# Optimization experiments

Hardware: AMD Instinct MI355X
Metric: run time of the kernel (lower is better)

## Reference

```python
import jax, jax.numpy as jnp
import numpy as np

B, T, V, D, P, DEP = 64, 32, 32000, 1024, 8, 4
TAU = 1.0
EPS = 1e-5


def setup_inputs() -> dict:
    key = jax.random.key(0)
    ks = jax.random.split(key, 9)
    s = 0.02
    x = jax.random.randint(ks[0], (B, T), 0, V)
    emb = jax.random.normal(ks[1], (V, D), jnp.float32) * s
    pos = jax.random.normal(ks[2], (T, D), jnp.float32) * s
    # primitive library: n_prims MLPs (Linear -> GELU -> Linear), stacked
    w1 = jax.random.normal(ks[3], (P, D, D), jnp.float32) * s
    b1 = jnp.zeros((P, D), jnp.float32)
    w2 = jax.random.normal(ks[4], (P, D, D), jnp.float32) * s
    b2 = jnp.zeros((P, D), jnp.float32)
    # one selector Linear(dim, n_prims) per depth
    sel_w = jax.random.normal(ks[5], (DEP, P, D), jnp.float32) * s
    sel_b = jnp.zeros((DEP, P), jnp.float32)
    ln_g = jnp.ones((D,), jnp.float32)
    ln_b = jnp.zeros((D,), jnp.float32)
    head_w = jax.random.normal(ks[6], (V, D), jnp.float32) * s
    # fixed gumbel noise (replaces torch's in-op sampling, kept deterministic)
    u = jax.random.uniform(ks[7], (DEP, B, P), jnp.float32, 1e-6, 1.0 - 1e-6)
    gumbel = -jnp.log(-jnp.log(u))
    return dict(x=x, emb=emb, pos=pos, w1=w1, b1=b1, w2=w2, b2=b2,
                sel_w=sel_w, sel_b=sel_b, ln_g=ln_g, ln_b=ln_b,
                head_w=head_w, gumbel=gumbel)


def reference(x, emb, pos, w1, b1, w2, b2, sel_w, sel_b, ln_g, ln_b, head_w, gumbel):
    h = emb[x] + pos[None, :x.shape[1], :]          # [B,T,D]
    div = jnp.float32(0.0)
    unif = jnp.float32(1.0 / P)
    for d in range(DEP):
        ctx = h.mean(axis=1)                         # [B,D]
        logits = ctx @ sel_w[d].T + sel_b[d]         # [B,P]
        weights = jax.nn.softmax((logits + gumbel[d]) / TAU, axis=-1)
        # all primitives over all tokens at once (grouped GEMM), no T loop
        u1 = jax.nn.gelu(jnp.einsum('btd,pde->btpe', h, w1) + b1, approximate=False)
        prim = jnp.einsum('btpe,pef->btpf', u1, w2) + b2   # [B,T,P,D]
        h = h + jnp.einsum('btpf,bp->btf', prim, weights)  # residual add
        avg = weights.mean(axis=0)                   # [P]
        # F.kl_div(avg.log(), uniform, reduction='sum')
        div = div + jnp.sum(unif * (jnp.log(unif) - jnp.log(avg)))
    mu = h.mean(-1, keepdims=True)
    var = ((h - mu) ** 2).mean(-1, keepdims=True)
    hn = (h - mu) * jax.lax.rsqrt(var + EPS) * ln_g + ln_b
    return hn @ head_w.T, div
```

## Files before the change

kernel.cpp:

```cpp
#include <hip/hip_runtime.h>
#include <hip/hip_bf16.h>
#include <math.h>

typedef __bf16 bf16x8 __attribute__((ext_vector_type(8)));
typedef float  f32x4  __attribute__((ext_vector_type(4)));

struct __align__(8) bf16x4s { __hip_bfloat16 a, b, c, d; };

__device__ __forceinline__ void gload_lds16(const void* g, void* l) {
  __builtin_amdgcn_global_load_lds(
      (const __attribute__((address_space(1))) void*)g,
      (__attribute__((address_space(3))) void*)l, 16, 0, 0);
}

__device__ __forceinline__ float fast_gelu(float v) {
  float s = 0.70710678118654752f * v;
  float a = fabsf(s);
  float t = __builtin_amdgcn_rcpf(fmaf(0.3275911f, a, 1.0f));
  float p = t * fmaf(t, fmaf(t, fmaf(t, fmaf(t, 1.061405429f, -1.453152027f),
                                     1.421413741f), -0.284496736f), 0.254829592f);
  float e = __expf(-a * a);
  float er = copysignf(fmaf(-p, e, 1.0f), s);
  return 0.5f * v * (1.0f + er);
}

#define BAR()   asm volatile("s_barrier" ::: "memory")
#define LGKM0() do { asm volatile("s_waitcnt lgkmcnt(0)" ::: "memory"); \
                     __builtin_amdgcn_sched_barrier(0); } while (0)
#define VMC(N)  do { asm volatile("s_waitcnt vmcnt(" #N ")" ::: "memory"); \
                     __builtin_amdgcn_sched_barrier(0); } while (0)
#define P1()    __builtin_amdgcn_s_setprio(1)
#define P0()    __builtin_amdgcn_s_setprio(0)

#define MQ(MB, NB, AV, BV)                                                    \
  do {                                                                        \
    _Pragma("unroll")                                                         \
    for (int mi_ = 0; mi_ < 4; ++mi_)                                         \
      _Pragma("unroll")                                                       \
      for (int nj_ = 0; nj_ < 2; ++nj_)                                       \
        _Pragma("unroll")                                                     \
        for (int kk_ = 0; kk_ < 2; ++kk_)                                     \
          acc[MB + mi_][NB + nj_] = __builtin_amdgcn_mfma_f32_16x16x32_bf16(  \
              AV[mi_][kk_], BV[nj_][kk_], acc[MB + mi_][NB + nj_], 0, 0, 0);  \
  } while (0)

template<int EPI>
__global__ __launch_bounds__(512, 2)
void gemm_nt(const __hip_bfloat16* __restrict__ A,
             const __hip_bfloat16* __restrict__ B,
             const int K, const int Kc, const int N,
             const float* __restrict__ p0,
             const float* __restrict__ p1,
             float* __restrict__ f32out,
             __hip_bfloat16* __restrict__ bfout)
{
  __shared__ __align__(16) __hip_bfloat16 lds[65536];

  const int tid = threadIdx.x;
  const int lane = tid & 63, wid = tid >> 6;
  const int l15 = lane & 15, l4 = lane >> 4;
  const int r8 = lane >> 3, blk = lane & 7;
  const int wm = wid >> 2, wn = wid & 3;

  const int nx = gridDim.x;
  const int flat = blockIdx.x + nx * blockIdx.y;
  const int q = (nx * gridDim.y) >> 3;
  const int nid = (flat & 7) * q + (flat >> 3);
  const long m0 = (long)(nid % nx) * 256;
  const long n0 = (long)(nid / nx) * 256;

  const int kbeg = blockIdx.z * Kc;
  const int nt = Kc / 64;

  f32x4 acc[8][4] = {};
  bf16x8 arE[4][2], arL[4][2], brE[2][2], brL[2][2];

  auto stageA = [&](int buf, int h, int k0) {
#pragma unroll
    for (int p2 = 0; p2 < 2; ++p2) {
      int ch = p2 * 16 + h * 8 + wid;
      int row = ch * 8 + r8;
      gload_lds16(A + (m0 + row) * (long)K + k0 + ((blk ^ r8) << 3),
                  lds + buf * 16384 + ch * 512);
    }
  };
  auto stageB = [&](int buf, int h, int k0) {
#pragma unroll
    for (int p2 = 0; p2 < 2; ++p2) {
      int ch = (p2 * 2 + (wid >> 2)) * 8 + h * 4 + (wid & 3);
      int row = ch * 8 + r8;
      gload_lds16(B + (n0 + row) * (long)K + k0 + ((blk ^ r8) << 3),
                  lds + 32768 + buf * 16384 + ch * 512);
    }
  };
  auto stage4 = [&](int buf, int k0) {
    stageA(buf, 0, k0); stageA(buf, 1, k0);
    stageB(buf, 0, k0); stageB(buf, 1, k0);
  };
  auto readAE = [&](int buf) {
    const __hip_bfloat16* pA = lds + buf * 16384;
#pragma unroll
    for (int mi = 0; mi < 4; ++mi)
#pragma unroll
      for (int kk = 0; kk < 2; ++kk) {
        int row = wm * 128 + mi * 16 + l15;
        arE[mi][kk] = *(const bf16x8*)(pA + row * 64 + (((kk * 4 + l4) ^ (row & 7)) << 3));
      }
  };
  auto readAL = [&](int buf) {
    const __hip_bfloat16* pA = lds + buf * 16384;
#pragma unroll
    for (int mi = 0; mi < 4; ++mi)
#pragma unroll
      for (int kk = 0; kk < 2; ++kk) {
        int row = wm * 128 + 64 + mi * 16 + l15;
        arL[mi][kk] = *(const bf16x8*)(pA + row * 64 + (((kk * 4 + l4) ^ (row & 7)) << 3));
      }
  };
  auto readBE = [&](int buf) {
    const __hip_bfloat16* pB = lds + 32768 + buf * 16384;
#pragma unroll
    for (int nj = 0; nj < 2; ++nj)
#pragma unroll
      for (int kk = 0; kk < 2; ++kk) {
        int row = wn * 64 + nj * 16 + l15;
        brE[nj][kk] = *(const bf16x8*)(pB + row * 64 + (((kk * 4 + l4) ^ (row & 7)) << 3));
      }
  };
  auto readBL = [&](int buf) {
    const __hip_bfloat16* pB = lds + 32768 + buf * 16384;
#pragma unroll
    for (int nj = 0; nj < 2; ++nj)
#pragma unroll
      for (int kk = 0; kk < 2; ++kk) {
        int row = wn * 64 + 32 + nj * 16 + l15;
        brL[nj][kk] = *(const bf16x8*)(pB + row * 64 + (((kk * 4 + l4) ^ (row & 7)) << 3));
      }
  };

  stage4(0, kbeg);
  stage4(1, kbeg + 64);
  VMC(8);
  BAR();
  readAE(0); readBE(0);

  for (int s = 0; s < nt; ++s) {
    const int b = s & 1;
    readBL(b); readAL(b);
    P1();
    MQ(0, 0, arE, brE);
    MQ(0, 2, arE, brL);
    MQ(4, 0, arL, brE);
    MQ(4, 2, arL, brL);
    P0();
    LGKM0();
    BAR();
    if (s + 2 < nt) {
      stage4(b, kbeg + (s + 2) * 64);
      VMC(8);
    } else if (s + 2 == nt) {
      VMC(0);
    }
    BAR();
    if (s + 1 < nt) { readAE(b ^ 1); readBE(b ^ 1); }
  }

  const long slab = (EPI == 2) ? (long)blockIdx.z * (long)(gridDim.x * 256) * N : 0;
#pragma unroll
  for (int mi = 0; mi < 8; ++mi) {
    const long gmb = m0 + wm * 128 + mi * 16 + l4 * 4;
    const int b = (int)(gmb >> 5);
#pragma unroll
    for (int nj = 0; nj < 4; ++nj) {
      const long gn = n0 + wn * 64 + nj * 16 + l15;
      if constexpr (EPI == 0) {
        const int p = (int)(gn >> 10), e = (int)(gn & 1023);
        const float bias = p0[(p << 10) + e];
        const float wpb = p1[(b << 3) + p];
#pragma unroll
        for (int r = 0; r < 4; ++r) {
          float v = fast_gelu(acc[mi][nj][r] + bias) * wpb;
          bfout[(gmb + r) * (long)N + gn] = __float2bfloat16(v);
        }
      } else {
#pragma unroll
        for (int r = 0; r < 4; ++r)
          f32out[slab + (gmb + r) * (long)N + gn] = acc[mi][nj][r];
      }
    }
  }
}

__global__ void cvt_bf16_k(const float* __restrict__ in, __hip_bfloat16* __restrict__ out, long n) {
  long i = ((long)blockIdx.x * blockDim.x + threadIdx.x) * 4;
  if (i >= n) return;
  float4 v = *(const float4*)(in + i);
  *(bf16x4s*)(out + i) = bf16x4s{__float2bfloat16(v.x), __float2bfloat16(v.y),
                                 __float2bfloat16(v.z), __float2bfloat16(v.w)};
}

__global__ void tconv_k(const float* __restrict__ in, __hip_bfloat16* __restrict__ out,
                        long in_bs, long out_rs, long out_bs) {
  __shared__ float tile[32][33];
  int p = blockIdx.z;
  int r0 = blockIdx.y * 32, c0 = blockIdx.x * 32;
  int tx = threadIdx.x, ty = threadIdx.y;
#pragma unroll
  for (int i = 0; i < 32; i += 8)
    tile[ty + i][tx] = in[(long)p * in_bs + (long)(r0 + ty + i) * 1024 + c0 + tx];
  __syncthreads();
#pragma unroll
  for (int i = 0; i < 32; i += 8)
    out[(long)(c0 + ty + i) * out_rs + (long)p * out_bs + (r0 + tx)] =
        __float2bfloat16(tile[tx][ty + i]);
}

__global__ void embed_k(const int* __restrict__ x, const float* __restrict__ emb,
                        const float* __restrict__ pos, float* __restrict__ h,
                        __hip_bfloat16* __restrict__ hb, float* __restrict__ divp) {
  int row = blockIdx.x;
  int t = row & 31;
  int c = threadIdx.x * 4;
  long tok = x[row];
  float4 e = *(const float4*)(emb + tok * 1024 + c);
  float4 q = *(const float4*)(pos + (long)t * 1024 + c);
  float4 v{e.x + q.x, e.y + q.y, e.z + q.z, e.w + q.w};
  *(float4*)(h + (long)row * 1024 + c) = v;
  *(bf16x4s*)(hb + (long)row * 1024 + c) =
      bf16x4s{__float2bfloat16(v.x), __float2bfloat16(v.y),
              __float2bfloat16(v.z), __float2bfloat16(v.w)};
  if (row == 0 && threadIdx.x == 0) *divp = 0.f;
}

__global__ void select_wb2_k(const float* __restrict__ h, const float* __restrict__ selw,
                             const float* __restrict__ selb, const float* __restrict__ gum,
                             const float* __restrict__ b2, float* __restrict__ W,
                             float* __restrict__ wb2, int dep) {
  int b = blockIdx.x, tid = threadIdx.x;
  int c = tid * 4;
  float4 s{0.f, 0.f, 0.f, 0.f};
  for (int t = 0; t < 32; ++t) {
    const float4 v = *(const float4*)(h + ((long)(b * 32 + t)) * 1024 + c);
    s.x += v.x; s.y += v.y; s.z += v.z; s.w += v.w;
  }
  float lp[8];
#pragma unroll
  for (int p = 0; p < 8; ++p) {
    const float4 w = *(const float4*)(selw + dep * 8192 + p * 1024 + c);
    lp[p] = (s.x * w.x + s.y * w.y + s.z * w.z + s.w * w.w) * (1.f / 32.f);
  }
  int lane = tid & 63, wid = tid >> 6;
#pragma unroll
  for (int p = 0; p < 8; ++p)
    for (int o = 32; o; o >>= 1) lp[p] += __shfl_down(lp[p], o);
  __shared__ float red[4][8];
  __shared__ float wsm[8];
  if (lane == 0) {
#pragma unroll
    for (int p = 0; p < 8; ++p) red[wid][p] = lp[p];
  }
  __syncthreads();
  if (tid == 0) {
    float lg[8], mx = -1e30f;
    for (int p = 0; p < 8; ++p) {
      lg[p] = red[0][p] + red[1][p] + red[2][p] + red[3][p]
            + selb[dep * 8 + p] + gum[dep * 512 + b * 8 + p];
      mx = fmaxf(mx, lg[p]);
    }
    float sm = 0.f;
    for (int p = 0; p < 8; ++p) { lg[p] = expf(lg[p] - mx); sm += lg[p]; }
    float inv = 1.f / sm;
    for (int p = 0; p < 8; ++p) { wsm[p] = lg[p] * inv; W[dep * 512 + b * 8 + p] = lg[p] * inv; }
  }
  __syncthreads();
  float4 a{0.f, 0.f, 0.f, 0.f};
#pragma unroll
  for (int p = 0; p < 8; ++p) {
    float wp = wsm[p];
    const float4 v = *(const float4*)(b2 + p * 1024 + c);
    a.x += wp * v.x; a.y += wp * v.y; a.z += wp * v.z; a.w += wp * v.w;
  }
  *(float4*)(wb2 + (long)b * 1024 + c) = a;
}

__global__ void h_update_k(const float* __restrict__ part, float* __restrict__ h,
                           const float* __restrict__ wb2, __hip_bfloat16* __restrict__ hb,
                           const float* __restrict__ Wd, float* __restrict__ divp) {
  int row = blockIdx.x;
  int c = threadIdx.x * 4;
  long idx = (long)row * 1024 + c;
  float4 a = *(const float4*)(h + idx);
  const float4 w = *(const float4*)(wb2 + (long)(row >> 5) * 1024 + c);
  a.x += w.x; a.y += w.y; a.z += w.z; a.w += w.w;
#pragma unroll
  for (int s = 0; s < 8; ++s) {
    const float4 v = *(const float4*)(part + (long)s * 2097152 + idx);
    a.x += v.x; a.y += v.y; a.z += v.z; a.w += v.w;
  }
  *(float4*)(h + idx) = a;
  *(bf16x4s*)(hb + idx) = bf16x4s{__float2bfloat16(a.x), __float2bfloat16(a.y),
                                  __float2bfloat16(a.z), __float2bfloat16(a.w)};
  if (blockIdx.x == 0 && threadIdx.x < 64) {
    float w8[8];
#pragma unroll
    for (int p = 0; p < 8; ++p) w8[p] = Wd[threadIdx.x * 8 + p];
#pragma unroll
    for (int p = 0; p < 8; ++p)
      for (int o = 32; o; o >>= 1) w8[p] += __shfl_down(w8[p], o);
    if (threadIdx.x == 0) {
      float d = *divp;
      const float u = 0.125f, lu = logf(0.125f);
#pragma unroll
      for (int p = 0; p < 8; ++p) d += u * (lu - logf(w8[p] * (1.f / 64.f)));
      *divp = d;
    }
  }
}

__global__ void ln_k(const float* __restrict__ h, const float* __restrict__ g,
                     const float* __restrict__ be, __hip_bfloat16* __restrict__ hnb,
                     const float* __restrict__ divp, float* __restrict__ divout) {
  int row = blockIdx.x, tid = threadIdx.x;
  int c = tid * 4;
  const float4 v = *(const float4*)(h + (long)row * 1024 + c);
  float s = v.x + v.y + v.z + v.w;
  float q = v.x * v.x + v.y * v.y + v.z * v.z + v.w * v.w;
  for (int o = 32; o; o >>= 1) { s += __shfl_down(s, o); q += __shfl_down(q, o); }
  __shared__ float red[16];
  int lane = tid & 63, wid = tid >> 6;
  if (lane == 0) { red[wid] = s; red[8 + wid] = q; }
  __syncthreads();
  if (tid == 0) {
    float S = red[0] + red[1] + red[2] + red[3];
    float Q = red[8] + red[9] + red[10] + red[11];
    float mu = S * (1.f / 1024.f);
    float var = Q * (1.f / 1024.f) - mu * mu;
    red[0] = mu; red[1] = rsqrtf(var + 1e-5f);
  }
  __syncthreads();
  float mu = red[0], rs = red[1];
  float4 gg = *(const float4*)(g + c), bb = *(const float4*)(be + c);
  *(bf16x4s*)(hnb + (long)row * 1024 + c) =
      bf16x4s{__float2bfloat16((v.x - mu) * rs * gg.x + bb.x),
              __float2bfloat16((v.y - mu) * rs * gg.y + bb.y),
              __float2bfloat16((v.z - mu) * rs * gg.z + bb.z),
              __float2bfloat16((v.w - mu) * rs * gg.w + bb.w)};
  if (row == 0 && tid == 0) *divout = *divp;
}

extern "C" void kernel_launch(void* const* d_in, const int* in_sizes, int n_in,
                              void* d_out, int out_size, void* d_ws, size_t ws_size,
                              hipStream_t stream) {
  (void)in_sizes; (void)n_in; (void)out_size; (void)ws_size;
  const int*   x     = (const int*)  d_in[0];
  const float* emb   = (const float*)d_in[1];
  const float* pos   = (const float*)d_in[2];
  const float* w1    = (const float*)d_in[3];
  const float* b1    = (const float*)d_in[4];
  const float* w2    = (const float*)d_in[5];
  const float* b2    = (const float*)d_in[6];
  const float* selw  = (const float*)d_in[7];
  const float* selb  = (const float*)d_in[8];
  const float* lng   = (const float*)d_in[9];
  const float* lnb   = (const float*)d_in[10];
  const float* headw = (const float*)d_in[11];
  const float* gum   = (const float*)d_in[12];
  float* out = (float*)d_out;

  char* ws = (char*)d_ws;
  __hip_bfloat16* w1t   = (__hip_bfloat16*)(ws);
  __hip_bfloat16* w2t   = (__hip_bfloat16*)(ws + 16777216);
  __hip_bfloat16* headb = (__hip_bfloat16*)(ws + 33554432);
  float*          h     = (float*)(ws + 99090432);
  __hip_bfloat16* hb    = (__hip_bfloat16*)(ws + 107479040);
  __hip_bfloat16* u1    = (__hip_bfloat16*)(ws + 111673344);
  float*          Wall  = (float*)(ws + 145227776);
  float*          wb2   = (float*)(ws + 145240064);
  float*          divp  = (float*)(ws + 145502208);
  float*          part  = out;

  cvt_bf16_k<<<32000, 256, 0, stream>>>(headw, headb, 32768000L);
  tconv_k<<<dim3(32, 32, 8), dim3(32, 8), 0, stream>>>(w1, w1t, 1L << 20, 1024L, 1L << 20);
  tconv_k<<<dim3(32, 32, 8), dim3(32, 8), 0, stream>>>(w2, w2t, 1L << 20, 8192L, 1024L);
  embed_k<<<2048, 256, 0, stream>>>(x, emb, pos, h, hb, divp);

  for (int d = 0; d < 4; ++d) {
    select_wb2_k<<<64, 256, 0, stream>>>(h, selw, selb, gum, b2, Wall, wb2, d);
    gemm_nt<0><<<dim3(8, 32), 512, 0, stream>>>(hb, w1t, 1024, 1024, 8192, b1, Wall + d * 512, nullptr, u1);
    gemm_nt<2><<<dim3(8, 4, 8), 512, 0, stream>>>(u1, w2t, 8192, 1024, 1024, nullptr, nullptr, part, nullptr);
    h_update_k<<<2048, 256, 0, stream>>>(part, h, wb2, hb, Wall + d * 512, divp);
  }

  ln_k<<<2048, 256, 0, stream>>>(h, lng, lnb, hb, divp, out + 65536000L);
  gemm_nt<2><<<dim3(8, 125), 512, 0, stream>>>(hb, headb, 1024, 1024, 32000, nullptr, nullptr, out, nullptr);
}
```

Before: 662.8 us.

## Interleave global-to-LDS staging with MFMA quadrants in an eight-phase unrolled loop

Restructures the GEMM main loop into a two-stage unrolled schedule. Each of the four MFMA quadrants is preceded by a fine-grained slice of the next tile's global-to-LDS loads and LDS reads, separated by barriers. The goal is to hide memory latency behind compute more evenly, in the style of hipBLASLt ping-pong schedules, instead of issuing all loads in one burst between compute blocks. It adds many more barriers and assumes nt is even, and the fine-grained buffer reuse ordering is easy to get wrong.

```diff
diff --git a/kernel.cpp b/kernel.cpp
--- a/kernel.cpp
+++ b/kernel.cpp
@@ -93,10 +93,6 @@
                   lds + 32768 + buf * 16384 + ch * 512);
     }
   };
-  auto stage4 = [&](int buf, int k0) {
-    stageA(buf, 0, k0); stageA(buf, 1, k0);
-    stageB(buf, 0, k0); stageB(buf, 1, k0);
-  };
   auto readAE = [&](int buf) {
     const __hip_bfloat16* pA = lds + buf * 16384;
 #pragma unroll
@@ -138,31 +134,58 @@
       }
   };
 
-  stage4(0, kbeg);
-  stage4(1, kbeg + 64);
-  VMC(8);
+  stageA(0, 0, kbeg); stageB(0, 0, kbeg); stageB(0, 1, kbeg); stageA(0, 1, kbeg);
+  VMC(4);
+  stageA(1, 0, kbeg + 64); stageB(1, 0, kbeg + 64); stageB(1, 1, kbeg + 64);
+  VMC(6);
   BAR();
-  readAE(0); readBE(0);
-
-  for (int s = 0; s < nt; ++s) {
-    const int b = s & 1;
-    readBL(b); readAL(b);
-    P1();
-    MQ(0, 0, arE, brE);
-    MQ(0, 2, arE, brL);
-    MQ(4, 0, arL, brE);
-    MQ(4, 2, arL, brL);
-    P0();
-    LGKM0();
-    BAR();
-    if (s + 2 < nt) {
-      stage4(b, kbeg + (s + 2) * 64);
-      VMC(8);
-    } else if (s + 2 == nt) {
-      VMC(0);
-    }
-    BAR();
-    if (s + 1 < nt) { readAE(b ^ 1); readBE(b ^ 1); }
+
+  const int nit = nt >> 1;
+  for (int t = 0; t < nit; ++t) {
+    const bool fl = (t + 1 < nit);
+    const int kA = kbeg + (2 * t + 1) * 64;
+    const int kB = kbeg + (2 * t + 2) * 64;
+    const int kC = kbeg + (2 * t + 3) * 64;
+    readAE(0); readBE(0);
+    stageA(1, 1, kA);
+    BAR(); LGKM0();
+    P1(); MQ(0, 0, arE, brE); P0();
+    BAR();
+    readBL(0);
+    if (fl) stageA(0, 0, kB);
+    BAR(); LGKM0();
+    P1(); MQ(0, 2, arE, brL); P0();
+    BAR();
+    readAL(0);
+    if (fl) stageB(0, 0, kB);
+    BAR(); LGKM0();
+    P1(); MQ(4, 0, arL, brE); P0();
+    BAR();
+    if (fl) stageB(0, 1, kB);
+    BAR();
+    P1(); MQ(4, 2, arL, brL); P0();
+    if (fl) { VMC(6); } else { VMC(0); }
+    BAR();
+    readAE(1); readBE(1);
+    if (fl) stageA(0, 1, kB);
+    BAR(); LGKM0();
+    P1(); MQ(0, 0, arE, brE); P0();
+    BAR();
+    readBL(1);
+    if (fl) stageA(1, 0, kC);
+    BAR(); LGKM0();
+    P1(); MQ(0, 2, arE, brL); P0();
+    BAR();
+    readAL(1);
+    if (fl) stageB(1, 0, kC);
+    BAR(); LGKM0();
+    P1(); MQ(4, 0, arL, brE); P0();
+    BAR();
+    if (fl) stageB(1, 1, kC);
+    BAR();
+    P1(); MQ(4, 2, arL, brL); P0();
+    if (fl) VMC(6);
+    BAR();
   }
 
   const long slab = (EPI == 2) ? (long)blockIdx.z * (long)(gridDim.x * 256) * N : 0;
```

Result: faster. 639.6 us (-3.5%).

## Load GEMM B operand directly to registers and store split-K partials in bf16

Applied to the files above, without the earlier changes.

The GEMM kernel now stages only the A tile through LDS, halving shared memory to 64KB. B fragments are loaded straight from global memory into double-buffered registers, and the K loop is unrolled by two. Split-K partial sums in the second MLP GEMM are written as bf16 instead of fp32, and h_update reads them as bf16, roughly halving that round-trip traffic. The cost is uncoalesced, per-lane global loads for B, higher register pressure at 2 blocks per CU, and reduced precision in the accumulated partials.

```diff
diff --git a/kernel.cpp b/kernel.cpp
--- a/kernel.cpp
+++ b/kernel.cpp
@@ -54,7 +54,7 @@
              float* __restrict__ f32out,
              __hip_bfloat16* __restrict__ bfout)
 {
-  __shared__ __align__(16) __hip_bfloat16 lds[65536];
+  __shared__ __align__(16) __hip_bfloat16 lds[32768];
 
   const int tid = threadIdx.x;
   const int lane = tid & 63, wid = tid >> 6;
@@ -73,29 +73,28 @@
   const int nt = Kc / 64;
 
   f32x4 acc[8][4] = {};
-  bf16x8 arE[4][2], arL[4][2], brE[2][2], brL[2][2];
-
-  auto stageA = [&](int buf, int h, int k0) {
-#pragma unroll
-    for (int p2 = 0; p2 < 2; ++p2) {
-      int ch = p2 * 16 + h * 8 + wid;
+  bf16x8 ar[4][2];
+  bf16x8 b0E[2][2], b0L[2][2], b1E[2][2], b1L[2][2];
+
+  auto stageA2 = [&](int buf, int k0) {
+#pragma unroll
+    for (int p2 = 0; p2 < 4; ++p2) {
+      int ch = p2 * 8 + wid;
       int row = ch * 8 + r8;
       gload_lds16(A + (m0 + row) * (long)K + k0 + ((blk ^ r8) << 3),
                   lds + buf * 16384 + ch * 512);
     }
   };
-  auto stageB = [&](int buf, int h, int k0) {
-#pragma unroll
-    for (int p2 = 0; p2 < 2; ++p2) {
-      int ch = (p2 * 2 + (wid >> 2)) * 8 + h * 4 + (wid & 3);
-      int row = ch * 8 + r8;
-      gload_lds16(B + (n0 + row) * (long)K + k0 + ((blk ^ r8) << 3),
-                  lds + 32768 + buf * 16384 + ch * 512);
-    }
-  };
-  auto stage4 = [&](int buf, int k0) {
-    stageA(buf, 0, k0); stageA(buf, 1, k0);
-    stageB(buf, 0, k0); stageB(buf, 1, k0);
+  auto loadB = [&](bf16x8 (&bE)[2][2], bf16x8 (&bL)[2][2], int k0) {
+#pragma unroll
+    for (int nj = 0; nj < 2; ++nj)
+#pragma unroll
+      for (int kk = 0; kk < 2; ++kk) {
+        bE[nj][kk] = *(const bf16x8*)(B + (n0 + wn * 64 + nj * 16 + l15) * (long)K
+                                        + k0 + kk * 32 + l4 * 8);
+        bL[nj][kk] = *(const bf16x8*)(B + (n0 + wn * 64 + 32 + nj * 16 + l15) * (long)K
+                                        + k0 + kk * 32 + l4 * 8);
+      }
   };
   auto readAE = [&](int buf) {
     const __hip_bfloat16* pA = lds + buf * 16384;
@@ -104,7 +103,7 @@
 #pragma unroll
       for (int kk = 0; kk < 2; ++kk) {
         int row = wm * 128 + mi * 16 + l15;
-        arE[mi][kk] = *(const bf16x8*)(pA + row * 64 + (((kk * 4 + l4) ^ (row & 7)) << 3));
+        ar[mi][kk] = *(const bf16x8*)(pA + row * 64 + (((kk * 4 + l4) ^ (row & 7)) << 3));
       }
   };
   auto readAL = [&](int buf) {
@@ -114,58 +113,53 @@
 #pragma unroll
       for (int kk = 0; kk < 2; ++kk) {
         int row = wm * 128 + 64 + mi * 16 + l15;
-        arL[mi][kk] = *(const bf16x8*)(pA + row * 64 + (((kk * 4 + l4) ^ (row & 7)) << 3));
+        ar[mi][kk] = *(const bf16x8*)(pA + row * 64 + (((kk * 4 + l4) ^ (row & 7)) << 3));
       }
   };
-  auto readBE = [&](int buf) {
-    const __hip_bfloat16* pB = lds + 32768 + buf * 16384;
-#pragma unroll
-    for (int nj = 0; nj < 2; ++nj)
-#pragma unroll
-      for (int kk = 0; kk < 2; ++kk) {
-        int row = wn * 64 + nj * 16 + l15;
-        brE[nj][kk] = *(const bf16x8*)(pB + row * 64 + (((kk * 4 + l4) ^ (row & 7)) << 3));
-      }
-  };
-  auto readBL = [&](int buf) {
-    const __hip_bfloat16* pB = lds + 32768 + buf * 16384;
-#pragma unroll
-    for (int nj = 0; nj < 2; ++nj)
-#pragma unroll
-      for (int kk = 0; kk < 2; ++kk) {
-        int row = wn * 64 + 32 + nj * 16 + l15;
-        brL[nj][kk] = *(const bf16x8*)(pB + row * 64 + (((kk * 4 + l4) ^ (row & 7)) << 3));
-      }
-  };
-
-  stage4(0, kbeg);
-  stage4(1, kbeg + 64);
+
+  stageA2(0, kbeg);
+  loadB(b0E, b0L, kbeg);
+  stageA2(1, kbeg + 64);
+  VMC(12);
+  BAR();
+  readAE(0);
+
+  const int nit = nt >> 1;
+  for (int t = 0; t < nit - 1; ++t) {
+    loadB(b1E, b1L, kbeg + (2 * t + 1) * 64);
+    P1(); MQ(0, 0, ar, b0E); MQ(0, 2, ar, b0L); P0();
+    readAL(0);
+    P1(); MQ(4, 0, ar, b0E); MQ(4, 2, ar, b0L); P0();
+    LGKM0();
+    BAR();
+    stageA2(0, kbeg + (2 * t + 2) * 64);
+    VMC(12);
+    BAR();
+    readAE(1);
+    loadB(b0E, b0L, kbeg + (2 * t + 2) * 64);
+    P1(); MQ(0, 0, ar, b1E); MQ(0, 2, ar, b1L); P0();
+    readAL(1);
+    P1(); MQ(4, 0, ar, b1E); MQ(4, 2, ar, b1L); P0();
+    LGKM0();
+    BAR();
+    stageA2(1, kbeg + (2 * t + 3) * 64);
+    VMC(12);
+    BAR();
+    readAE(0);
+  }
+
+  loadB(b1E, b1L, kbeg + (nt - 1) * 64);
+  P1(); MQ(0, 0, ar, b0E); MQ(0, 2, ar, b0L); P0();
+  readAL(0);
+  P1(); MQ(4, 0, ar, b0E); MQ(4, 2, ar, b0L); P0();
   VMC(8);
   BAR();
-  readAE(0); readBE(0);
-
-  for (int s = 0; s < nt; ++s) {
-    const int b = s & 1;
-    readBL(b); readAL(b);
-    P1();
-    MQ(0, 0, arE, brE);
-    MQ(0, 2, arE, brL);
-    MQ(4, 0, arL, brE);
-    MQ(4, 2, arL, brL);
-    P0();
-    LGKM0();
-    BAR();
-    if (s + 2 < nt) {
-      stage4(b, kbeg + (s + 2) * 64);
-      VMC(8);
-    } else if (s + 2 == nt) {
-      VMC(0);
-    }
-    BAR();
-    if (s + 1 < nt) { readAE(b ^ 1); readBE(b ^ 1); }
-  }
-
-  const long slab = (EPI == 2) ? (long)blockIdx.z * (long)(gridDim.x * 256) * N : 0;
+  readAE(1);
+  P1(); MQ(0, 0, ar, b1E); MQ(0, 2, ar, b1L); P0();
+  readAL(1);
+  P1(); MQ(4, 0, ar, b1E); MQ(4, 2, ar, b1L); P0();
+
+  const long slab = (EPI == 4) ? (long)blockIdx.z * (long)(gridDim.x * 256) * N : 0;
 #pragma unroll
   for (int mi = 0; mi < 8; ++mi) {
     const long gmb = m0 + wm * 128 + mi * 16 + l4 * 4;
@@ -182,10 +176,14 @@
           float v = fast_gelu(acc[mi][nj][r] + bias) * wpb;
           bfout[(gmb + r) * (long)N + gn] = __float2bfloat16(v);
         }
+      } else if constexpr (EPI == 2) {
+#pragma unroll
+        for (int r = 0; r < 4; ++r)
+          f32out[(gmb + r) * (long)N + gn] = acc[mi][nj][r];
       } else {
 #pragma unroll
         for (int r = 0; r < 4; ++r)
-          f32out[slab + (gmb + r) * (long)N + gn] = acc[mi][nj][r];
+          bfout[slab + (gmb + r) * (long)N + gn] = __float2bfloat16(acc[mi][nj][r]);
       }
     }
   }
@@ -283,7 +281,7 @@
   *(float4*)(wb2 + (long)b * 1024 + c) = a;
 }
 
-__global__ void h_update_k(const float* __restrict__ part, float* __restrict__ h,
+__global__ void h_update_k(const __hip_bfloat16* __restrict__ part, float* __restrict__ h,
                            const float* __restrict__ wb2, __hip_bfloat16* __restrict__ hb,
                            const float* __restrict__ Wd, float* __restrict__ divp) {
   int row = blockIdx.x;
@@ -294,8 +292,9 @@
   a.x += w.x; a.y += w.y; a.z += w.z; a.w += w.w;
 #pragma unroll
   for (int s = 0; s < 8; ++s) {
-    const float4 v = *(const float4*)(part + (long)s * 2097152 + idx);
-    a.x += v.x; a.y += v.y; a.z += v.z; a.w += v.w;
+    const bf16x4s v = *(const bf16x4s*)(part + (long)s * 2097152 + idx);
+    a.x += __bfloat162float(v.a); a.y += __bfloat162float(v.b);
+    a.z += __bfloat162float(v.c); a.w += __bfloat162float(v.d);
   }
   *(float4*)(h + idx) = a;
   *(bf16x4s*)(hb + idx) = bf16x4s{__float2bfloat16(a.x), __float2bfloat16(a.y),
@@ -377,7 +376,7 @@
   float*          Wall  = (float*)(ws + 145227776);
   float*          wb2   = (float*)(ws + 145240064);
   float*          divp  = (float*)(ws + 145502208);
-  float*          part  = out;
+  __hip_bfloat16* part  = (__hip_bfloat16*)out;
 
   cvt_bf16_k<<<32000, 256, 0, stream>>>(headw, headb, 32768000L);
   tconv_k<<<dim3(32, 32, 8), dim3(32, 8), 0, stream>>>(w1, w1t, 1L << 20, 1024L, 1L << 20);
@@ -387,7 +386,7 @@
   for (int d = 0; d < 4; ++d) {
     select_wb2_k<<<64, 256, 0, stream>>>(h, selw, selb, gum, b2, Wall, wb2, d);
     gemm_nt<0><<<dim3(8, 32), 512, 0, stream>>>(hb, w1t, 1024, 1024, 8192, b1, Wall + d * 512, nullptr, u1);
-    gemm_nt<2><<<dim3(8, 4, 8), 512, 0, stream>>>(u1, w2t, 8192, 1024, 1024, nullptr, nullptr, part, nullptr);
+    gemm_nt<4><<<dim3(8, 4, 8), 512, 0, stream>>>(u1, w2t, 8192, 1024, 1024, nullptr, nullptr, nullptr, part);
     h_update_k<<<2048, 256, 0, stream>>>(part, h, wb2, hb, Wall + d * 512, divp);
   }
 
```

New measurement: 822.0 us. 24.0% more time.
